# Kernel optimization log

Measured on AMD Instinct MI355X. Metric: run time of the kernel, lower is better.

The kernel has to match this reference:

```python
import jax, jax.numpy as jnp
import numpy as np
from jax import lax

BATCH, SEQ, IN_F, H_SIZE, OUT_F = 65536, 64, 16, 10, 5

def setup_inputs() -> dict:
    key = jax.random.key(0)
    k1, k2, k3, k4, k5 = jax.random.split(key, 5)
    x = jax.random.uniform(k1, (BATCH, SEQ, IN_F), dtype=jnp.float32)
    W1 = jax.random.normal(k2, (IN_F, H_SIZE), dtype=jnp.float32) * (1.0 / np.sqrt(IN_F))
    b1 = jax.random.normal(k3, (H_SIZE,), dtype=jnp.float32) * 0.02
    W2 = jax.random.normal(k4, (H_SIZE, OUT_F), dtype=jnp.float32) * (1.0 / np.sqrt(H_SIZE))
    b2 = jax.random.normal(k5, (OUT_F,), dtype=jnp.float32) * 0.02
    return {"x": x, "W1": W1, "b1": b1, "W2": W2, "b2": b2}

def reference(x, W1, b1, W2, b2):
    # h_{t} = tanh(h_{t-1} + x_t @ W1 + b1); y = sigmoid(h_T @ W2 + b2)
    b = x.shape[0]
    h0 = jnp.zeros((b, W1.shape[1]), dtype=x.dtype)
    # precompute all input projections in one big GEMM: [B,S,H]
    a = jnp.einsum('bsi,ih->bsh', x, W1) + b1
    def step(h, a_t):
        return jnp.tanh(h + a_t), None
    h, _ = lax.scan(step, h0, jnp.swapaxes(a, 0, 1))  # scan over seq
    return jax.nn.sigmoid(h @ W2 + b2)
```

## Files before the change

### kernel.cpp

```cpp
#include <hip/hip_runtime.h>

#define BATCH 65536
#define SEQ   64
#define INF   16
#define HS    10
#define UPL   3
#define OUTF  5

#define PIN(v) asm volatile("" : "+v"(v))

__device__ __forceinline__ float4 shfl_xor4(float4 v, int m) {
    return make_float4(__shfl_xor(v.x, m), __shfl_xor(v.y, m),
                       __shfl_xor(v.z, m), __shfl_xor(v.w, m));
}

__global__ __launch_bounds__(256, 4) void rnn_fused(
    const float* __restrict__ x,  const float* __restrict__ W1,
    const float* __restrict__ b1, const float* __restrict__ W2,
    const float* __restrict__ b2, float* __restrict__ out)
{
    const int g   = blockIdx.x * 256 + threadIdx.x;
    const int row = g >> 2;
    const int j   = g & 3;

    float wl[4][4][UPL];
    float bl[UPL];
#pragma unroll
    for (int u = 0; u < UPL; ++u) {
        const int hu = UPL * j + u;
        const int hc = (hu < HS) ? hu : 0;
        const bool ok = (hu < HS);
        bl[u] = ok ? b1[hc] : 0.0f;
#pragma unroll
        for (int m = 0; m < 4; ++m) {
            const int lm = j ^ m;
#pragma unroll
            for (int k = 0; k < 4; ++k) {
                const int col = 4 * lm + k;
                wl[m][k][u] = ok ? W1[col * HS + hc] : 0.0f;
            }
        }
    }
#pragma unroll
    for (int m = 0; m < 4; ++m)
#pragma unroll
        for (int k = 0; k < 4; ++k)
#pragma unroll
            for (int u = 0; u < UPL; ++u) { PIN(wl[m][k][u]); }
#pragma unroll
    for (int u = 0; u < UPL; ++u) { PIN(bl[u]); }

    float h[UPL];
#pragma unroll
    for (int u = 0; u < UPL; ++u) h[u] = 0.0f;

    const float4* __restrict__ xr =
        reinterpret_cast<const float4*>(x) + (size_t)row * (SEQ * 4) + j;

    float4 buf[4];
#pragma unroll
    for (int r = 0; r < 4; ++r) buf[r] = xr[r * 4];

#pragma unroll 4
    for (int s = 0; s < SEQ; ++s) {
        const int slot = s & 3;
        const float4 g0 = buf[slot];
        const int pf = (s + 4 < SEQ) ? (s + 4) : (SEQ - 1);
        buf[slot] = xr[pf * 4];

        const float4 g1 = shfl_xor4(g0, 1);
        const float4 g2 = shfl_xor4(g0, 2);
        const float4 g3 = shfl_xor4(g0, 3);

#pragma unroll
        for (int u = 0; u < UPL; ++u) {
            float p0 = fmaf(g0.x, wl[0][0][u], bl[u]);
            p0 = fmaf(g0.y, wl[0][1][u], p0);
            p0 = fmaf(g0.z, wl[0][2][u], p0);
            p0 = fmaf(g0.w, wl[0][3][u], p0);
            float p1 = g1.x * wl[1][0][u];
            p1 = fmaf(g1.y, wl[1][1][u], p1);
            p1 = fmaf(g1.z, wl[1][2][u], p1);
            p1 = fmaf(g1.w, wl[1][3][u], p1);
            float p2 = g2.x * wl[2][0][u];
            p2 = fmaf(g2.y, wl[2][1][u], p2);
            p2 = fmaf(g2.z, wl[2][2][u], p2);
            p2 = fmaf(g2.w, wl[2][3][u], p2);
            float p3 = g3.x * wl[3][0][u];
            p3 = fmaf(g3.y, wl[3][1][u], p3);
            p3 = fmaf(g3.z, wl[3][2][u], p3);
            p3 = fmaf(g3.w, wl[3][3][u], p3);
            const float a = (p0 + p1) + (p2 + p3);

            const float t = h[u] + a;
            const float e = __expf(t + t);
            h[u] = fmaf(-2.0f, __builtin_amdgcn_rcpf(e + 1.0f), 1.0f);
        }
    }

    float y[OUTF];
#pragma unroll
    for (int o = 0; o < OUTF; ++o) y[o] = 0.0f;
#pragma unroll
    for (int u = 0; u < UPL; ++u) {
        const int hu = UPL * j + u;
        const float* w2r = W2 + (size_t)((hu < HS) ? hu : 0) * OUTF;
#pragma unroll
        for (int o = 0; o < OUTF; ++o)
            y[o] = fmaf(h[u], w2r[o], y[o]);
    }
#pragma unroll
    for (int o = 0; o < OUTF; ++o) y[o] += __shfl_xor(y[o], 1);
#pragma unroll
    for (int o = 0; o < OUTF; ++o) y[o] += __shfl_xor(y[o], 2);
#pragma unroll
    for (int o = 0; o < OUTF; ++o)
        y[o] = __builtin_amdgcn_rcpf(1.0f + __expf(-(y[o] + b2[o])));

    float* op = out + (size_t)row * OUTF;
    op[j] = y[j];
    if (j == 0) op[4] = y[4];
}

extern "C" void kernel_launch(void* const* d_in, const int* in_sizes, int n_in,
                              void* d_out, int out_size, void* d_ws, size_t ws_size,
                              hipStream_t stream) {
    const float* x  = (const float*)d_in[0];
    const float* W1 = (const float*)d_in[1];
    const float* b1 = (const float*)d_in[2];
    const float* W2 = (const float*)d_in[3];
    const float* b2 = (const float*)d_in[4];
    float* out = (float*)d_out;

    rnn_fused<<<(BATCH * 4) / 256, 256, 0, stream>>>(x, W1, b1, W2, b2, out);
}
```

Baseline: 379.2 us.

## Use DPP quad permutes, prescale weights for exp2 tanh, peel prefetch tail

Replaces ds_bpermute-based __shfl_xor lane exchanges with DPP quad_perm moves for both the per-step input sharing and the final reduction. Folds the 2*log2(e) factor into W1 and b1 so each tanh step is a single fma plus a native exp2, with no scaling multiplies. The last four sequence steps are peeled so the prefetch needs no clamped index or redundant load. These changes aim to cut LDS-crossbar latency and ALU work on the serial recurrence path. The cost is reliance on DPP builtins and slightly different rounding.

```diff
diff --git a/kernel.cpp b/kernel.cpp
--- a/kernel.cpp
+++ b/kernel.cpp
@@ -6,12 +6,19 @@
 #define HS    10
 #define UPL   3
 #define OUTF  5
+#define KSC   2.8853900817779268f
 
 #define PIN(v) asm volatile("" : "+v"(v))
 
-__device__ __forceinline__ float4 shfl_xor4(float4 v, int m) {
-    return make_float4(__shfl_xor(v.x, m), __shfl_xor(v.y, m),
-                       __shfl_xor(v.z, m), __shfl_xor(v.w, m));
+template <int C>
+__device__ __forceinline__ float qp(float v) {
+    return __builtin_bit_cast(float,
+        __builtin_amdgcn_update_dpp(0, __builtin_bit_cast(int, v),
+                                    C, 0xF, 0xF, true));
+}
+template <int C>
+__device__ __forceinline__ float4 qp4(float4 v) {
+    return make_float4(qp<C>(v.x), qp<C>(v.y), qp<C>(v.z), qp<C>(v.w));
 }
 
 __global__ __launch_bounds__(256, 4) void rnn_fused(
@@ -30,14 +37,14 @@
         const int hu = UPL * j + u;
         const int hc = (hu < HS) ? hu : 0;
         const bool ok = (hu < HS);
-        bl[u] = ok ? b1[hc] : 0.0f;
+        bl[u] = ok ? KSC * b1[hc] : 0.0f;
 #pragma unroll
         for (int m = 0; m < 4; ++m) {
             const int lm = j ^ m;
 #pragma unroll
             for (int k = 0; k < 4; ++k) {
                 const int col = 4 * lm + k;
-                wl[m][k][u] = ok ? W1[col * HS + hc] : 0.0f;
+                wl[m][k][u] = ok ? KSC * W1[col * HS + hc] : 0.0f;
             }
         }
     }
@@ -61,42 +68,45 @@
 #pragma unroll
     for (int r = 0; r < 4; ++r) buf[r] = xr[r * 4];
 
+#define STEP(S, PF)                                                          \
+    {                                                                        \
+        const int slot = (S) & 3;                                            \
+        const float4 g0 = buf[slot];                                         \
+        if (PF) buf[slot] = xr[((S) + 4) * 4];                               \
+        const float4 g1 = qp4<0xB1>(g0);                                     \
+        const float4 g2 = qp4<0x4E>(g0);                                     \
+        const float4 g3 = qp4<0x1B>(g0);                                     \
+        _Pragma("unroll")                                                    \
+        for (int u = 0; u < UPL; ++u) {                                      \
+                \
+            float p0 = fmaf(g0.x, wl[0][0][u], bl[u]);                       \
+            p0 = fmaf(g0.y, wl[0][1][u], p0);                                \
+            p0 = fmaf(g0.z, wl[0][2][u], p0);                                \
+            p0 = fmaf(g0.w, wl[0][3][u], p0);                                \
+            float p1 = g1.x * wl[1][0][u];                                   \
+            p1 = fmaf(g1.y, wl[1][1][u], p1);                                \
+            p1 = fmaf(g1.z, wl[1][2][u], p1);                                \
+            p1 = fmaf(g1.w, wl[1][3][u], p1);                                \
+            float p2 = g2.x * wl[2][0][u];                                   \
+            p2 = fmaf(g2.y, wl[2][1][u], p2);                                \
+            p2 = fmaf(g2.z, wl[2][2][u], p2);                                \
+            p2 = fmaf(g2.w, wl[2][3][u], p2);                                \
+            float p3 = g3.x * wl[3][0][u];                                   \
+            p3 = fmaf(g3.y, wl[3][1][u], p3);                                \
+            p3 = fmaf(g3.z, wl[3][2][u], p3);                                \
+            p3 = fmaf(g3.w, wl[3][3][u], p3);                                \
+            const float aK = (p0 + p1) + (p2 + p3);     \
+                  \
+            const float e = __builtin_amdgcn_exp2f(fmaf(KSC, h[u], aK));     \
+            h[u] = fmaf(-2.0f, __builtin_amdgcn_rcpf(e + 1.0f), 1.0f);       \
+        }                                                                    \
+    }
+
 #pragma unroll 4
-    for (int s = 0; s < SEQ; ++s) {
-        const int slot = s & 3;
-        const float4 g0 = buf[slot];
-        const int pf = (s + 4 < SEQ) ? (s + 4) : (SEQ - 1);
-        buf[slot] = xr[pf * 4];
-
-        const float4 g1 = shfl_xor4(g0, 1);
-        const float4 g2 = shfl_xor4(g0, 2);
-        const float4 g3 = shfl_xor4(g0, 3);
-
+    for (int s = 0; s < SEQ - 4; ++s) STEP(s, true);
 #pragma unroll
-        for (int u = 0; u < UPL; ++u) {
-            float p0 = fmaf(g0.x, wl[0][0][u], bl[u]);
-            p0 = fmaf(g0.y, wl[0][1][u], p0);
-            p0 = fmaf(g0.z, wl[0][2][u], p0);
-            p0 = fmaf(g0.w, wl[0][3][u], p0);
-            float p1 = g1.x * wl[1][0][u];
-            p1 = fmaf(g1.y, wl[1][1][u], p1);
-            p1 = fmaf(g1.z, wl[1][2][u], p1);
-            p1 = fmaf(g1.w, wl[1][3][u], p1);
-            float p2 = g2.x * wl[2][0][u];
-            p2 = fmaf(g2.y, wl[2][1][u], p2);
-            p2 = fmaf(g2.z, wl[2][2][u], p2);
-            p2 = fmaf(g2.w, wl[2][3][u], p2);
-            float p3 = g3.x * wl[3][0][u];
-            p3 = fmaf(g3.y, wl[3][1][u], p3);
-            p3 = fmaf(g3.z, wl[3][2][u], p3);
-            p3 = fmaf(g3.w, wl[3][3][u], p3);
-            const float a = (p0 + p1) + (p2 + p3);
-
-            const float t = h[u] + a;
-            const float e = __expf(t + t);
-            h[u] = fmaf(-2.0f, __builtin_amdgcn_rcpf(e + 1.0f), 1.0f);
-        }
-    }
+    for (int s = SEQ - 4; s < SEQ; ++s) STEP(s, false);
+#undef STEP
 
     float y[OUTF];
 #pragma unroll
@@ -110,9 +120,9 @@
             y[o] = fmaf(h[u], w2r[o], y[o]);
     }
 #pragma unroll
-    for (int o = 0; o < OUTF; ++o) y[o] += __shfl_xor(y[o], 1);
+    for (int o = 0; o < OUTF; ++o) y[o] += qp<0xB1>(y[o]);
 #pragma unroll
-    for (int o = 0; o < OUTF; ++o) y[o] += __shfl_xor(y[o], 2);
+    for (int o = 0; o < OUTF; ++o) y[o] += qp<0x4E>(y[o]);
 #pragma unroll
     for (int o = 0; o < OUTF; ++o)
         y[o] = __builtin_amdgcn_rcpf(1.0f + __expf(-(y[o] + b2[o])));
```

Result: slower. 387.1 us (+2.1%).
